# Performance work log

Measured on AMD Instinct MI355X. Metric: run time of the kernel, lower is better.

## Reference

```python
import jax, jax.numpy as jnp
import numpy as np

NUM_HEADS = 2
LN_EPS = 1e-5
NEG_MASK = -1e9


def setup_inputs() -> dict:
    key = jax.random.key(0)
    ks = jax.random.split(key, 8)
    B, C, T, N = 8, 64, 32, 400
    H, D = NUM_HEADS, C // NUM_HEADS
    s = 1.0 / np.sqrt(C)
    return {
        "x": jax.random.normal(ks[0], (B, C, T, N), dtype=jnp.float32),
        "Wq": jax.random.normal(ks[1], (C, C), dtype=jnp.float32) * s,
        "Wk": jax.random.normal(ks[2], (C, C), dtype=jnp.float32) * s,
        "Wv": jax.random.normal(ks[3], (C, C), dtype=jnp.float32) * s,
        "a_src": jax.random.normal(ks[4], (H, D), dtype=jnp.float32) * 0.1,
        "a_dst": jax.random.normal(ks[5], (H, D), dtype=jnp.float32) * 0.1,
        "ln_gamma": jnp.ones((C,), dtype=jnp.float32),
        "ln_beta": jnp.zeros((C,), dtype=jnp.float32),
        "gso": jax.random.randint(ks[6], (N, N), 0, 2, dtype=jnp.int32),
    }


def reference(x, Wq, Wk, Wv, a_src, a_dst, ln_gamma, ln_beta, gso):
    B, C, T, N = x.shape
    H = NUM_HEADS
    D = C // H
    # (B,C,T,N) -> (B*T, N, C)
    xr = jnp.transpose(x, (0, 2, 3, 1)).reshape(B * T, N, C)
    # torch Linear: y = x @ W.T; then split heads -> (BT, N, H, D)
    Q = (xr @ Wq.T).reshape(B * T, N, H, D)
    K = (xr @ Wk.T).reshape(B * T, N, H, D)
    V = (xr @ Wv.T).reshape(B * T, N, H, D)
    # GAT additive scores per head
    s_src = jnp.einsum("bnhd,hd->bnh", Q, a_src)  # (BT, N, H)
    s_dst = jnp.einsum("bnhd,hd->bnh", K, a_dst)  # (BT, N, H)
    scores = s_src[:, :, None, :] + s_dst[:, None, :, :]  # (BT, i, j, H)
    scores = jax.nn.leaky_relu(scores, negative_slope=0.2)
    mask = jnp.where(gso == 0, jnp.float32(NEG_MASK), 0.0)  # (N, N)
    scores = scores + mask[None, :, :, None]
    attn = jax.nn.softmax(scores, axis=2)  # softmax over dst j; dropout = identity (eval)
    out = jnp.einsum("bijh,bjhd->bihd", attn, V).reshape(B * T, N, C)
    # LayerNorm over channel dim
    mu = jnp.mean(out, axis=-1, keepdims=True)
    var = jnp.var(out, axis=-1, keepdims=True)
    out = (out - mu) * jax.lax.rsqrt(var + LN_EPS) * ln_gamma + ln_beta
    # (BT, N, C) -> (B, C, T, N)
    return jnp.transpose(out.reshape(B, T, N, C), (0, 3, 1, 2))
```

## Files before the change

### kernel.cpp

```cpp
#include <hip/hip_runtime.h>
#include <hip/hip_bf16.h>

typedef __attribute__((ext_vector_type(8))) short bf16x8;
typedef __attribute__((ext_vector_type(4))) float f32x4;
typedef __attribute__((ext_vector_type(4))) int i32x4;
typedef __attribute__((ext_vector_type(4))) unsigned int u32x4;
typedef __attribute__((ext_vector_type(2))) unsigned int u32x2;

#define B_   8
#define C_   64
#define T_   32
#define N_   400
#define BT_  256
#define NKT_ 13
#define CN_  12800
#define VROW 424
#define WROW 72
#define L2E_ 1.4426950408889634f
#define SH6_ (-8.656170245333780f)

#if __has_builtin(__builtin_amdgcn_exp2f)
#define EXP2F(x) __builtin_amdgcn_exp2f(x)
#else
#define EXP2F(x) __expf((x) * 0.6931471805599453f)
#endif

__global__ __launch_bounds__(256) void gat_prep(
    const int* __restrict__ gso, unsigned int* __restrict__ mb)
{
  int idx = blockIdx.x*256 + threadIdx.x;
  if (idx < N_*16) {
    int i = idx >> 4, kw = idx & 15;
    unsigned int bits = 0;
    if (kw < 13) {
      int j0 = kw * 32;
      #pragma unroll
      for (int bb = 0; bb < 32; ++bb) {
        int j = j0 + bb;
        if (j < N_ && gso[i*N_ + j] != 0) bits |= (1u << bb);
      }
    }
    mb[idx] = bits;
  }
}

__global__ __launch_bounds__(1024) void gat_fused(
    const float* __restrict__ x, const float* __restrict__ Wq,
    const float* __restrict__ Wk, const float* __restrict__ Wv,
    const float* __restrict__ a_src, const float* __restrict__ a_dst,
    const float* __restrict__ gamma, const float* __restrict__ beta,
    const unsigned int* __restrict__ mb, float* __restrict__ out)
{
  __shared__ __align__(16) __hip_bfloat16 Vt[64][VROW];
  __shared__ __align__(16) __hip_bfloat16 wvb[80][WROW];
  __shared__ __align__(16) float e1d_s[2][416];
  __shared__ __align__(16) float e2d_s[2][416];
  __shared__ __align__(16) float si_s[2][400];
  __shared__ __align__(16) float ob[128][68];
  __shared__ __align__(16) unsigned int lut_s[16][2];
  __shared__ float g_s[64], b_s[64];

  const int tid = threadIdx.x;
  const int bt = blockIdx.x;
  const int b = bt >> 5, t = bt & 31;
  const int lane = tid & 63, wave = tid >> 6;
  const int col = lane & 15, quad = lane >> 4;

  #pragma unroll
  for (int it = 0; it < 4; ++it) {
    int idx = it*1024 + tid;
    int o = idx >> 6, c = idx & 63;
    wvb[o][c] = __float2bfloat16(Wv[o*C_ + c]);
  }
  if (tid < 256) {
    int ww = tid >> 6, c = tid & 63, h = ww >> 1;
    const float* W = (ww & 1) ? Wk : Wq;
    const float* a = (ww & 1) ? a_dst : a_src;
    float s = 0.f;
    #pragma unroll
    for (int d = 0; d < 32; ++d) s += W[(h*32 + d)*C_ + c] * a[h*32 + d];
    wvb[64 + ww][c] = __float2bfloat16(s * L2E_);
  } else if (tid < 320) {
    g_s[tid - 256] = gamma[tid - 256];
  } else if (tid < 384) {
    b_s[tid - 320] = beta[tid - 320];
  } else if (tid < 448) {
    int tt = tid - 384;
    int h = (tt >> 4) & 1, cc = 400 + (tt & 15);
    if (tt < 32) e1d_s[h][cc] = 0.f; else e2d_s[h][cc] = 0.f;
  } else if (tid < 464) {
    int n = tid - 448;
    lut_s[n][0] = ((n & 1) ? 0x0000FFFFu : 0u) | ((n & 2) ? 0xFFFF0000u : 0u);
    lut_s[n][1] = ((n & 4) ? 0x0000FFFFu : 0u) | ((n & 8) ? 0xFFFF0000u : 0u);
  }
  for (int idx = tid; idx < 12*WROW; idx += 1024)
    wvb[68 + idx/WROW][idx % WROW] = __float2bfloat16(0.f);
  for (int idx = tid; idx < 64*24; idx += 1024)
    Vt[idx/24][400 + idx%24] = __float2bfloat16(0.f);
  __syncthreads();

  {
    const float* xbase = x + ((size_t)b*C_*T_ + t)*N_;
    for (int nt = wave; nt < 25; nt += 16) {
      const int n0 = nt*16;
      bf16x8 bfrag[2];
      #pragma unroll
      for (int kt = 0; kt < 2; ++kt) {
        const float* xc = xbase + (size_t)(kt*32 + quad*8)*CN_ + n0 + col;
        union { short s[8]; bf16x8 v; } pk;
        #pragma unroll
        for (int j = 0; j < 8; ++j) {
          union { __hip_bfloat16 h; short s; } cv;
          cv.h = __float2bfloat16(xc[(size_t)j*CN_]);
          pk.s[j] = cv.s;
        }
        bfrag[kt] = pk.v;
      }
      #pragma unroll
      for (int ot = 0; ot < 5; ++ot) {
        f32x4 acc = {0.f, 0.f, 0.f, 0.f};
        #pragma unroll
        for (int kt = 0; kt < 2; ++kt) {
          bf16x8 afr = *(const bf16x8*)&wvb[ot*16 + col][kt*32 + quad*8];
          acc = __builtin_amdgcn_mfma_f32_16x16x32_bf16(afr, bfrag[kt], acc, 0, 0, 0);
        }
        if (ot < 4) {
          #pragma unroll
          for (int r = 0; r < 4; ++r)
            Vt[ot*16 + quad*4 + r][n0 + col] = __float2bfloat16(acc[r]);
        } else if (quad == 0) {
          #pragma unroll
          for (int r = 0; r < 4; ++r) {
            int h = r >> 1;
            if (r & 1) {
              e1d_s[h][n0 + col] = EXP2F(acc[r] + SH6_);
              e2d_s[h][n0 + col] = EXP2F(fmaf(0.2f, acc[r], SH6_));
            } else {
              si_s[h][n0 + col] = acc[r];
            }
          }
        }
      }
    }
  }
  __syncthreads();

  const int hh = wave & 1, itile = wave >> 1;
  const int rowA = col;
  const unsigned int qsh = quad * 8;

  bf16x8 ones;
  #pragma unroll
  for (int k = 0; k < 8; ++k) ones[k] = (short)0x3F80;

  for (int r0 = 0; r0 < N_; r0 += 128) {
    const int ibase = r0 + itile*16;
    if (ibase < N_) {
      const int irow = ibase + rowA;
      const float si1 = si_s[hh][irow];
      const float E1i = EXP2F(si1 + SH6_);
      const float E2i = EXP2F(fmaf(0.2f, si1, SH6_));
      const u32x4* mp = (const u32x4*)(mb + irow*16);
      u32x4 mw0 = mp[0], mw1 = mp[1], mw2 = mp[2];
      unsigned int mw12 = mb[irow*16 + 12];
      const float* e1p = e1d_s[hh] + quad*8;
      const float* e2p = e2d_s[hh] + quad*8;
      const __hip_bfloat16* v0p = &Vt[hh*32 + rowA][quad*8];
      const __hip_bfloat16* v1p = v0p + 16*VROW;

      f32x4 d0 = {0,0,0,0}, d1 = {0,0,0,0}, d2 = {0,0,0,0};
      #pragma unroll
      for (int kt = 0; kt < NKT_; ++kt) {
        unsigned int mword = (kt < 4) ? mw0[kt] : (kt < 8) ? mw1[kt-4]
                           : (kt < 12) ? mw2[kt-8] : mw12;
        unsigned int mbyte = (mword >> qsh) & 0xffu;
        u32x2 mlo = *(const u32x2*)&lut_s[mbyte & 15u][0];
        u32x2 mhi = *(const u32x2*)&lut_s[mbyte >> 4][0];
        f32x4 x1a = *(const f32x4*)(e1p + kt*32);
        f32x4 x1b = *(const f32x4*)(e1p + kt*32 + 4);
        f32x4 x2a = *(const f32x4*)(e2p + kt*32);
        f32x4 x2b = *(const f32x4*)(e2p + kt*32 + 4);
        bf16x8 vb0 = *(const bf16x8*)(v0p + kt*32);
        bf16x8 vb1 = *(const bf16x8*)(v1p + kt*32);
        unsigned int eu[8];
        #pragma unroll
        for (int jj = 0; jj < 8; ++jj) {
          float f1 = (jj < 4) ? x1a[jj] : x1b[jj-4];
          float f2 = (jj < 4) ? x2a[jj] : x2b[jj-4];
          eu[jj] = __float_as_uint(fmaxf(E1i * f1, E2i * f2));
        }
        union { i32x4 i; bf16x8 v; } af;
        af.i.x = (int)(__builtin_amdgcn_perm(eu[1], eu[0], 0x07060302u) & mlo.x);
        af.i.y = (int)(__builtin_amdgcn_perm(eu[3], eu[2], 0x07060302u) & mlo.y);
        af.i.z = (int)(__builtin_amdgcn_perm(eu[5], eu[4], 0x07060302u) & mhi.x);
        af.i.w = (int)(__builtin_amdgcn_perm(eu[7], eu[6], 0x07060302u) & mhi.y);
        d0 = __builtin_amdgcn_mfma_f32_16x16x32_bf16(af.v, vb0, d0, 0, 0, 0);
        d1 = __builtin_amdgcn_mfma_f32_16x16x32_bf16(af.v, vb1, d1, 0, 0, 0);
        d2 = __builtin_amdgcn_mfma_f32_16x16x32_bf16(af.v, ones, d2, 0, 0, 0);
      }
      #pragma unroll
      for (int r = 0; r < 4; ++r) {
        float li = 1.0f / d2[r];
        int rl = itile*16 + quad*4 + r;
        ob[rl][hh*32 + rowA]      = d0[r] * li;
        ob[rl][hh*32 + 16 + rowA] = d1[r] * li;
      }
    }
    __syncthreads();

    {
      int rl = tid >> 3, cgi = tid & 7;
      int n = r0 + rl;
      if (n < N_) {
        float u[8]; float s = 0.f;
        #pragma unroll
        for (int k = 0; k < 8; ++k) { u[k] = ob[rl][cgi*8 + k]; s += u[k]; }
        s += __shfl_xor(s,1); s += __shfl_xor(s,2); s += __shfl_xor(s,4);
        float mu = s * (1.f/64.f);
        float q = 0.f;
        #pragma unroll
        for (int k = 0; k < 8; ++k) { float dv = u[k]-mu; q = fmaf(dv,dv,q); }
        q += __shfl_xor(q,1); q += __shfl_xor(q,2); q += __shfl_xor(q,4);
        float rstd = rsqrtf(q*(1.f/64.f) + 1e-5f);
        #pragma unroll
        for (int k = 0; k < 8; ++k)
          ob[rl][cgi*8 + k] = (u[k]-mu)*rstd*g_s[cgi*8 + k] + b_s[cgi*8 + k];
      }
    }
    __syncthreads();

    #pragma unroll
    for (int it = 0; it < 8; ++it) {
      int idx = it*1024 + tid;
      int c = idx >> 7, nn = idx & 127;
      int n = r0 + nn;
      if (n < N_) out[((size_t)(b*C_ + c)*T_ + t)*N_ + n] = ob[nn][c];
    }
    __syncthreads();
  }
}

extern "C" void kernel_launch(void* const* d_in, const int* in_sizes, int n_in,
                              void* d_out, int out_size, void* d_ws, size_t ws_size,
                              hipStream_t stream) {
  (void)in_sizes; (void)n_in; (void)out_size; (void)ws_size;
  const float* x     = (const float*)d_in[0];
  const float* Wq    = (const float*)d_in[1];
  const float* Wk    = (const float*)d_in[2];
  const float* Wv    = (const float*)d_in[3];
  const float* a_src = (const float*)d_in[4];
  const float* a_dst = (const float*)d_in[5];
  const float* gamma = (const float*)d_in[6];
  const float* beta  = (const float*)d_in[7];
  const int*   gso   = (const int*)d_in[8];
  float* out = (float*)d_out;

  unsigned int* mbp = (unsigned int*)d_ws;

  gat_prep<<<26, 256, 0, stream>>>(gso, mbp);
  gat_fused<<<BT_, 1024, 0, stream>>>(x, Wq, Wk, Wv, a_src, a_dst,
                                      gamma, beta, mbp, out);
}
```

Before: 115.9 us.

## Process all four row groups per wave to reuse V and score loads

The attention loop now handles all four 128-row groups inside a single k-loop, so each V fragment and dst-score vector loaded from LDS serves four MFMA groups instead of one. The bitmask is re-laid out in 16-row blocks so each lane reads its mask word with a coalesced stride per k-tile. The exp products use packed two-wide float multiplies. This raises register pressure, with twelve accumulator vectors live per wave, and moves the output writes into a second loop that still runs LayerNorm per group.

```diff
diff --git a/kernel.cpp b/kernel.cpp
--- a/kernel.cpp
+++ b/kernel.cpp
@@ -3,6 +3,7 @@
 
 typedef __attribute__((ext_vector_type(8))) short bf16x8;
 typedef __attribute__((ext_vector_type(4))) float f32x4;
+typedef __attribute__((ext_vector_type(2))) float f32x2;
 typedef __attribute__((ext_vector_type(4))) int i32x4;
 typedef __attribute__((ext_vector_type(4))) unsigned int u32x4;
 typedef __attribute__((ext_vector_type(2))) unsigned int u32x2;
@@ -16,6 +17,7 @@
 #define CN_  12800
 #define VROW 424
 #define WROW 72
+#define MROW 208
 #define L2E_ 1.4426950408889634f
 #define SH6_ (-8.656170245333780f)
 
@@ -26,21 +28,21 @@
 #endif
 
 __global__ __launch_bounds__(256) void gat_prep(
-    const int* __restrict__ gso, unsigned int* __restrict__ mb)
+    const int* __restrict__ gso, unsigned int* __restrict__ mbT)
 {
   int idx = blockIdx.x*256 + threadIdx.x;
-  if (idx < N_*16) {
-    int i = idx >> 4, kw = idx & 15;
+  if (idx < 25*MROW) {
+    int iblk = idx / MROW, rem = idx - iblk*MROW;
+    int kw = rem >> 4, ilo = rem & 15;
+    int i = iblk*16 + ilo;
     unsigned int bits = 0;
-    if (kw < 13) {
-      int j0 = kw * 32;
-      #pragma unroll
-      for (int bb = 0; bb < 32; ++bb) {
-        int j = j0 + bb;
-        if (j < N_ && gso[i*N_ + j] != 0) bits |= (1u << bb);
-      }
-    }
-    mb[idx] = bits;
+    int j0 = kw * 32;
+    #pragma unroll
+    for (int bb = 0; bb < 32; ++bb) {
+      int j = j0 + bb;
+      if (j < N_ && gso[i*N_ + j] != 0) bits |= (1u << bb);
+    }
+    mbT[idx] = bits;
   }
 }
 
@@ -49,7 +51,7 @@
     const float* __restrict__ Wk, const float* __restrict__ Wv,
     const float* __restrict__ a_src, const float* __restrict__ a_dst,
     const float* __restrict__ gamma, const float* __restrict__ beta,
-    const unsigned int* __restrict__ mb, float* __restrict__ out)
+    const unsigned int* __restrict__ mbT, float* __restrict__ out)
 {
   __shared__ __align__(16) __hip_bfloat16 Vt[64][VROW];
   __shared__ __align__(16) __hip_bfloat16 wvb[80][WROW];
@@ -153,57 +155,78 @@
   #pragma unroll
   for (int k = 0; k < 8; ++k) ones[k] = (short)0x3F80;
 
-  for (int r0 = 0; r0 < N_; r0 += 128) {
-    const int ibase = r0 + itile*16;
-    if (ibase < N_) {
-      const int irow = ibase + rowA;
-      const float si1 = si_s[hh][irow];
-      const float E1i = EXP2F(si1 + SH6_);
-      const float E2i = EXP2F(fmaf(0.2f, si1, SH6_));
-      const u32x4* mp = (const u32x4*)(mb + irow*16);
-      u32x4 mw0 = mp[0], mw1 = mp[1], mw2 = mp[2];
-      unsigned int mw12 = mb[irow*16 + 12];
-      const float* e1p = e1d_s[hh] + quad*8;
-      const float* e2p = e2d_s[hh] + quad*8;
-      const __hip_bfloat16* v0p = &Vt[hh*32 + rowA][quad*8];
-      const __hip_bfloat16* v1p = v0p + 16*VROW;
-
-      f32x4 d0 = {0,0,0,0}, d1 = {0,0,0,0}, d2 = {0,0,0,0};
-      #pragma unroll
-      for (int kt = 0; kt < NKT_; ++kt) {
-        unsigned int mword = (kt < 4) ? mw0[kt] : (kt < 8) ? mw1[kt-4]
-                           : (kt < 12) ? mw2[kt-8] : mw12;
+  f32x4 d0[4], d1[4], d2[4];
+  float E1[4], E2[4];
+  bool act[4];
+  const unsigned int* mpg[4];
+
+  #pragma unroll
+  for (int g = 0; g < 4; ++g) {
+    int ib = g*128 + itile*16;
+    act[g] = (g < 3) | (itile == 0);
+    int ir = act[g] ? (ib + rowA) : 0;
+    mpg[g] = mbT + (act[g] ? (ib >> 4)*MROW : 0) + rowA;
+    float si1 = si_s[hh][ir];
+    E1[g] = act[g] ? EXP2F(si1 + SH6_) : 0.f;
+    E2[g] = act[g] ? EXP2F(fmaf(0.2f, si1, SH6_)) : 0.f;
+    d0[g] = (f32x4){0,0,0,0}; d1[g] = (f32x4){0,0,0,0}; d2[g] = (f32x4){0,0,0,0};
+  }
+
+  {
+    const float* e1p = e1d_s[hh] + quad*8;
+    const float* e2p = e2d_s[hh] + quad*8;
+    const __hip_bfloat16* v0p = &Vt[hh*32 + rowA][quad*8];
+    const __hip_bfloat16* v1p = v0p + 16*VROW;
+
+    #pragma unroll
+    for (int kt = 0; kt < NKT_; ++kt) {
+      union { f32x4 v4[2]; f32x2 v2[4]; } u1, u2;
+      u1.v4[0] = *(const f32x4*)(e1p + kt*32);
+      u1.v4[1] = *(const f32x4*)(e1p + kt*32 + 4);
+      u2.v4[0] = *(const f32x4*)(e2p + kt*32);
+      u2.v4[1] = *(const f32x4*)(e2p + kt*32 + 4);
+      bf16x8 vb0 = *(const bf16x8*)(v0p + kt*32);
+      bf16x8 vb1 = *(const bf16x8*)(v1p + kt*32);
+
+      #pragma unroll
+      for (int g = 0; g < 4; ++g) {
+        unsigned int mword = mpg[g][kt*16];
         unsigned int mbyte = (mword >> qsh) & 0xffu;
         u32x2 mlo = *(const u32x2*)&lut_s[mbyte & 15u][0];
         u32x2 mhi = *(const u32x2*)&lut_s[mbyte >> 4][0];
-        f32x4 x1a = *(const f32x4*)(e1p + kt*32);
-        f32x4 x1b = *(const f32x4*)(e1p + kt*32 + 4);
-        f32x4 x2a = *(const f32x4*)(e2p + kt*32);
-        f32x4 x2b = *(const f32x4*)(e2p + kt*32 + 4);
-        bf16x8 vb0 = *(const bf16x8*)(v0p + kt*32);
-        bf16x8 vb1 = *(const bf16x8*)(v1p + kt*32);
-        unsigned int eu[8];
-        #pragma unroll
-        for (int jj = 0; jj < 8; ++jj) {
-          float f1 = (jj < 4) ? x1a[jj] : x1b[jj-4];
-          float f2 = (jj < 4) ? x2a[jj] : x2b[jj-4];
-          eu[jj] = __float_as_uint(fmaxf(E1i * f1, E2i * f2));
+        f32x2 e1g = {E1[g], E1[g]};
+        f32x2 e2g = {E2[g], E2[g]};
+        u32x2 w[4];
+        #pragma unroll
+        for (int q2 = 0; q2 < 4; ++q2) {
+          f32x2 a = e1g * u1.v2[q2];
+          f32x2 c = e2g * u2.v2[q2];
+          f32x2 m = {fmaxf(a.x, c.x), fmaxf(a.y, c.y)};
+          union { f32x2 f; u32x2 u; } cvt; cvt.f = m;
+          w[q2] = cvt.u;
         }
         union { i32x4 i; bf16x8 v; } af;
-        af.i.x = (int)(__builtin_amdgcn_perm(eu[1], eu[0], 0x07060302u) & mlo.x);
-        af.i.y = (int)(__builtin_amdgcn_perm(eu[3], eu[2], 0x07060302u) & mlo.y);
-        af.i.z = (int)(__builtin_amdgcn_perm(eu[5], eu[4], 0x07060302u) & mhi.x);
-        af.i.w = (int)(__builtin_amdgcn_perm(eu[7], eu[6], 0x07060302u) & mhi.y);
-        d0 = __builtin_amdgcn_mfma_f32_16x16x32_bf16(af.v, vb0, d0, 0, 0, 0);
-        d1 = __builtin_amdgcn_mfma_f32_16x16x32_bf16(af.v, vb1, d1, 0, 0, 0);
-        d2 = __builtin_amdgcn_mfma_f32_16x16x32_bf16(af.v, ones, d2, 0, 0, 0);
-      }
+        af.i.x = (int)(__builtin_amdgcn_perm(w[0].y, w[0].x, 0x07060302u) & mlo.x);
+        af.i.y = (int)(__builtin_amdgcn_perm(w[1].y, w[1].x, 0x07060302u) & mlo.y);
+        af.i.z = (int)(__builtin_amdgcn_perm(w[2].y, w[2].x, 0x07060302u) & mhi.x);
+        af.i.w = (int)(__builtin_amdgcn_perm(w[3].y, w[3].x, 0x07060302u) & mhi.y);
+        d0[g] = __builtin_amdgcn_mfma_f32_16x16x32_bf16(af.v, vb0, d0[g], 0, 0, 0);
+        d1[g] = __builtin_amdgcn_mfma_f32_16x16x32_bf16(af.v, vb1, d1[g], 0, 0, 0);
+        d2[g] = __builtin_amdgcn_mfma_f32_16x16x32_bf16(af.v, ones, d2[g], 0, 0, 0);
+      }
+    }
+  }
+
+  #pragma unroll
+  for (int p = 0; p < 4; ++p) {
+    const int r0 = p*128;
+    if (act[p]) {
       #pragma unroll
       for (int r = 0; r < 4; ++r) {
-        float li = 1.0f / d2[r];
+        float li = 1.0f / d2[p][r];
         int rl = itile*16 + quad*4 + r;
-        ob[rl][hh*32 + rowA]      = d0[r] * li;
-        ob[rl][hh*32 + 16 + rowA] = d1[r] * li;
+        ob[rl][hh*32 + rowA]      = d0[p][r] * li;
+        ob[rl][hh*32 + 16 + rowA] = d1[p][r] * li;
       }
     }
     __syncthreads();
@@ -255,9 +278,9 @@
   const int*   gso   = (const int*)d_in[8];
   float* out = (float*)d_out;
 
-  unsigned int* mbp = (unsigned int*)d_ws;
-
-  gat_prep<<<26, 256, 0, stream>>>(gso, mbp);
+  unsigned int* mbT = (unsigned int*)d_ws;
+
+  gat_prep<<<21, 256, 0, stream>>>(gso, mbT);
   gat_fused<<<BT_, 1024, 0, stream>>>(x, Wq, Wk, Wv, a_src, a_dst,
-                                      gamma, beta, mbp, out);
+                                      gamma, beta, mbT, out);
 }
```

Measured after the change: 123.6 us. +6.6%, slower.

## Prefetch x before weight setup, pack exp multiplies, narrow ob padding

Applied to the files above, without the earlier changes.

The first projection tile's x values are now loaded into registers at kernel start, so the global load latency overlaps the weight conversion and the first barrier. The strided tile loop becomes an explicit first tile plus a second tile for waves below 9. The inner attention loop computes the exp products as float2 vectors so the compiler can emit packed multiplies. The output staging row width changes from 68 to 65 floats to alter LDS bank mapping, which gives up 16-byte row alignment and adds register pressure from the prefetched values.

```diff
diff --git a/kernel.cpp b/kernel.cpp
--- a/kernel.cpp
+++ b/kernel.cpp
@@ -3,6 +3,7 @@
 
 typedef __attribute__((ext_vector_type(8))) short bf16x8;
 typedef __attribute__((ext_vector_type(4))) float f32x4;
+typedef __attribute__((ext_vector_type(2))) float f32x2;
 typedef __attribute__((ext_vector_type(4))) int i32x4;
 typedef __attribute__((ext_vector_type(4))) unsigned int u32x4;
 typedef __attribute__((ext_vector_type(2))) unsigned int u32x2;
@@ -16,6 +17,7 @@
 #define CN_  12800
 #define VROW 424
 #define WROW 72
+#define OBW  65
 #define L2E_ 1.4426950408889634f
 #define SH6_ (-8.656170245333780f)
 
@@ -56,7 +58,7 @@
   __shared__ __align__(16) float e1d_s[2][416];
   __shared__ __align__(16) float e2d_s[2][416];
   __shared__ __align__(16) float si_s[2][400];
-  __shared__ __align__(16) float ob[128][68];
+  __shared__ __align__(16) float ob[128][OBW];
   __shared__ __align__(16) unsigned int lut_s[16][2];
   __shared__ float g_s[64], b_s[64];
 
@@ -65,6 +67,18 @@
   const int b = bt >> 5, t = bt & 31;
   const int lane = tid & 63, wave = tid >> 6;
   const int col = lane & 15, quad = lane >> 4;
+
+  const float* xbase = x + ((size_t)b*C_*T_ + t)*N_;
+  float xf0[2][8];
+  {
+    const int n0 = wave*16;
+    #pragma unroll
+    for (int kt = 0; kt < 2; ++kt) {
+      const float* xc = xbase + (size_t)(kt*32 + quad*8)*CN_ + n0 + col;
+      #pragma unroll
+      for (int j = 0; j < 8; ++j) xf0[kt][j] = xc[(size_t)j*CN_];
+    }
+  }
 
   #pragma unroll
   for (int it = 0; it < 4; ++it) {
@@ -100,18 +114,15 @@
   __syncthreads();
 
   {
-    const float* xbase = x + ((size_t)b*C_*T_ + t)*N_;
-    for (int nt = wave; nt < 25; nt += 16) {
-      const int n0 = nt*16;
+    auto proj_tile = [&](int n0, const float xf[2][8]) {
       bf16x8 bfrag[2];
       #pragma unroll
       for (int kt = 0; kt < 2; ++kt) {
-        const float* xc = xbase + (size_t)(kt*32 + quad*8)*CN_ + n0 + col;
         union { short s[8]; bf16x8 v; } pk;
         #pragma unroll
         for (int j = 0; j < 8; ++j) {
           union { __hip_bfloat16 h; short s; } cv;
-          cv.h = __float2bfloat16(xc[(size_t)j*CN_]);
+          cv.h = __float2bfloat16(xf[kt][j]);
           pk.s[j] = cv.s;
         }
         bfrag[kt] = pk.v;
@@ -141,6 +152,19 @@
           }
         }
       }
+    };
+
+    proj_tile(wave*16, xf0);
+    if (wave < 9) {
+      float xf1[2][8];
+      const int n0 = (wave + 16)*16;
+      #pragma unroll
+      for (int kt = 0; kt < 2; ++kt) {
+        const float* xc = xbase + (size_t)(kt*32 + quad*8)*CN_ + n0 + col;
+        #pragma unroll
+        for (int j = 0; j < 8; ++j) xf1[kt][j] = xc[(size_t)j*CN_];
+      }
+      proj_tile(n0, xf1);
     }
   }
   __syncthreads();
@@ -167,6 +191,8 @@
       const float* e2p = e2d_s[hh] + quad*8;
       const __hip_bfloat16* v0p = &Vt[hh*32 + rowA][quad*8];
       const __hip_bfloat16* v1p = v0p + 16*VROW;
+      const f32x2 e1g = {E1i, E1i};
+      const f32x2 e2g = {E2i, E2i};
 
       f32x4 d0 = {0,0,0,0}, d1 = {0,0,0,0}, d2 = {0,0,0,0};
       #pragma unroll
@@ -176,24 +202,27 @@
         unsigned int mbyte = (mword >> qsh) & 0xffu;
         u32x2 mlo = *(const u32x2*)&lut_s[mbyte & 15u][0];
         u32x2 mhi = *(const u32x2*)&lut_s[mbyte >> 4][0];
-        f32x4 x1a = *(const f32x4*)(e1p + kt*32);
-        f32x4 x1b = *(const f32x4*)(e1p + kt*32 + 4);
-        f32x4 x2a = *(const f32x4*)(e2p + kt*32);
-        f32x4 x2b = *(const f32x4*)(e2p + kt*32 + 4);
+        union { f32x4 v4[2]; f32x2 v2[4]; } u1, u2;
+        u1.v4[0] = *(const f32x4*)(e1p + kt*32);
+        u1.v4[1] = *(const f32x4*)(e1p + kt*32 + 4);
+        u2.v4[0] = *(const f32x4*)(e2p + kt*32);
+        u2.v4[1] = *(const f32x4*)(e2p + kt*32 + 4);
         bf16x8 vb0 = *(const bf16x8*)(v0p + kt*32);
         bf16x8 vb1 = *(const bf16x8*)(v1p + kt*32);
-        unsigned int eu[8];
-        #pragma unroll
-        for (int jj = 0; jj < 8; ++jj) {
-          float f1 = (jj < 4) ? x1a[jj] : x1b[jj-4];
-          float f2 = (jj < 4) ? x2a[jj] : x2b[jj-4];
-          eu[jj] = __float_as_uint(fmaxf(E1i * f1, E2i * f2));
+        u32x2 w[4];
+        #pragma unroll
+        for (int q2 = 0; q2 < 4; ++q2) {
+          f32x2 a = e1g * u1.v2[q2];
+          f32x2 c = e2g * u2.v2[q2];
+          f32x2 m = {fmaxf(a.x, c.x), fmaxf(a.y, c.y)};
+          union { f32x2 f; u32x2 u; } cvt; cvt.f = m;
+          w[q2] = cvt.u;
         }
         union { i32x4 i; bf16x8 v; } af;
-        af.i.x = (int)(__builtin_amdgcn_perm(eu[1], eu[0], 0x07060302u) & mlo.x);
-        af.i.y = (int)(__builtin_amdgcn_perm(eu[3], eu[2], 0x07060302u) & mlo.y);
-        af.i.z = (int)(__builtin_amdgcn_perm(eu[5], eu[4], 0x07060302u) & mhi.x);
-        af.i.w = (int)(__builtin_amdgcn_perm(eu[7], eu[6], 0x07060302u) & mhi.y);
+        af.i.x = (int)(__builtin_amdgcn_perm(w[0].y, w[0].x, 0x07060302u) & mlo.x);
+        af.i.y = (int)(__builtin_amdgcn_perm(w[1].y, w[1].x, 0x07060302u) & mlo.y);
+        af.i.z = (int)(__builtin_amdgcn_perm(w[2].y, w[2].x, 0x07060302u) & mhi.x);
+        af.i.w = (int)(__builtin_amdgcn_perm(w[3].y, w[3].x, 0x07060302u) & mhi.y);
         d0 = __builtin_amdgcn_mfma_f32_16x16x32_bf16(af.v, vb0, d0, 0, 0, 0);
         d1 = __builtin_amdgcn_mfma_f32_16x16x32_bf16(af.v, vb1, d1, 0, 0, 0);
         d2 = __builtin_amdgcn_mfma_f32_16x16x32_bf16(af.v, ones, d2, 0, 0, 0);
```

Measured after the change: 117.3 us. Within noise of the previous version (+1.2%).
